# Kernel optimization log

Hardware: AMD Instinct MI355X
Metric: run time of the kernel (lower is better)

The kernel has to match this reference:

```python
import jax, jax.numpy as jnp
import numpy as np

EMBED_DIM = 192
NUM_HEADS = 4
HEAD_DIM = EMBED_DIM // NUM_HEADS
SCALE = HEAD_DIM ** -0.5


def setup_inputs() -> dict:
    key = jax.random.key(0)
    k_x, k_wqkv, k_bqkv, k_wp, k_bp = jax.random.split(key, 5)
    B, P, N, d = 8, 4, 1024, EMBED_DIM
    x = jax.random.normal(k_x, (B, P, N, d), dtype=jnp.float32)
    # torch Linear: y = x @ W.T + b, W shape [out, in]
    w_qkv = jax.random.normal(k_wqkv, (3 * d, d), dtype=jnp.float32) * (d ** -0.5)
    b_qkv = jax.random.normal(k_bqkv, (3 * d,), dtype=jnp.float32) * 0.02
    w_proj = jax.random.normal(k_wp, (d, d), dtype=jnp.float32) * (d ** -0.5)
    b_proj = jax.random.normal(k_bp, (d,), dtype=jnp.float32) * 0.02
    return {"x": x, "w_qkv": w_qkv, "b_qkv": b_qkv, "w_proj": w_proj, "b_proj": b_proj}


def reference(x, w_qkv, b_qkv, w_proj, b_proj):
    B, P, N, d = x.shape
    H, D = NUM_HEADS, HEAD_DIM
    qkv = jnp.einsum('bpnd,ed->bpne', x, w_qkv) + b_qkv  # [B,P,N,3d]
    q, k, v = jnp.split(qkv, 3, axis=-1)
    # split heads -> [B,P,H,N,D]
    split = lambda t: t.reshape(B, P, N, H, D).transpose(0, 1, 3, 2, 4)
    q, k, v = split(q), split(k), split(v)
    attn = jnp.einsum('bphnd,bphmd->bphnm', q, k) * SCALE
    attn = jax.nn.softmax(attn, axis=-1)
    z = jnp.einsum('bphnm,bphmd->bphnd', attn, v)
    z = z.transpose(0, 1, 3, 2, 4).reshape(B, P, N, H * D)
    z = jnp.einsum('bpnd,ed->bpne', z, w_proj) + b_proj
    return z
```

## Files before the change

### kernel.cpp

```cpp
#include <hip/hip_runtime.h>
#include <hip/hip_bf16.h>
#include <cstdint>
#include <cstddef>

typedef __attribute__((ext_vector_type(8))) short bf16x8;
typedef __attribute__((ext_vector_type(4))) float floatx4;
typedef __attribute__((ext_vector_type(16))) float floatx16;

#define SCALE_L2E 0.20823560929138437f

#define BPH 128
#define SEQ 1024
#define DMODEL 192
#define DHEAD 48
#define MROWS 32768
#define RESCALE_THR 11.5f

#define ZERO16 {0.f,0.f,0.f,0.f,0.f,0.f,0.f,0.f,0.f,0.f,0.f,0.f,0.f,0.f,0.f,0.f}

__device__ __forceinline__ unsigned short bfu(float f) {
    return __bfloat16_as_ushort(__float2bfloat16(f));
}
__device__ __forceinline__ unsigned pk2(float lo, float hi) {
    return (unsigned)bfu(lo) | ((unsigned)bfu(hi) << 16);
}

__global__ __launch_bounds__(256) void qkv_kernel(
    const float* __restrict__ x,
    const float* __restrict__ w_qkv,
    const float* __restrict__ b_qkv,
    unsigned short* __restrict__ q_ws,
    unsigned short* __restrict__ k_ws,
    unsigned short* __restrict__ vt_ws)
{
    __shared__ unsigned short a_lds[64 * 200];
    __shared__ unsigned short w_lds[64 * 200];
    const int t = threadIdx.x;
    const int m0 = blockIdx.x * 64;
    const int n0 = blockIdx.y * 64;

    #pragma unroll
    for (int i = 0; i < 12; ++i) {
        int idx = t + i * 256;
        int row = idx / 48, c4 = idx % 48;
        float4 v = *reinterpret_cast<const float4*>(x + (size_t)(m0 + row) * DMODEL + c4 * 4);
        unsigned short* dst = &a_lds[row * 200 + c4 * 4];
        dst[0] = bfu(v.x); dst[1] = bfu(v.y); dst[2] = bfu(v.z); dst[3] = bfu(v.w);
    }
    #pragma unroll
    for (int i = 0; i < 12; ++i) {
        int idx = t + i * 256;
        int row = idx / 48, c4 = idx % 48;
        float4 v = *reinterpret_cast<const float4*>(w_qkv + (size_t)(n0 + row) * DMODEL + c4 * 4);
        unsigned short* dst = &w_lds[row * 200 + c4 * 4];
        dst[0] = bfu(v.x); dst[1] = bfu(v.y); dst[2] = bfu(v.z); dst[3] = bfu(v.w);
    }
    __syncthreads();

    const int lane = t & 63, w = t >> 6;
    const int lrow = lane & 15, lhi = lane >> 4;

    floatx4 zf = {0.f, 0.f, 0.f, 0.f};
    floatx4 acc[4] = {zf, zf, zf, zf};

    #pragma unroll
    for (int ks = 0; ks < 6; ++ks) {
        bf16x8 af = *reinterpret_cast<const bf16x8*>(&a_lds[(w * 16 + lrow) * 200 + ks * 32 + lhi * 8]);
        #pragma unroll
        for (int cb = 0; cb < 4; ++cb) {
            bf16x8 bfr = *reinterpret_cast<const bf16x8*>(&w_lds[(cb * 16 + lrow) * 200 + ks * 32 + lhi * 8]);
            acc[cb] = __builtin_amdgcn_mfma_f32_16x16x32_bf16(af, bfr, acc[cb], 0, 0, 0);
        }
    }

    const int sec = n0 / 192;
    if (sec == 2) {
        __syncthreads();
        #pragma unroll
        for (int cb = 0; cb < 4; ++cb) {
            float bias = b_qkv[n0 + cb * 16 + lrow];
            #pragma unroll
            for (int r = 0; r < 4; ++r)
                a_lds[(cb * 16 + lrow) * 72 + (w * 16 + lhi * 4 + r)] = bfu(acc[cb][r] + bias);
        }
        __syncthreads();
        const int bp = m0 >> 10, nb = m0 & 1023;
        #pragma unroll
        for (int i = 0; i < 2; ++i) {
            int ch = t + i * 256;
            int c_local = ch >> 3, seg = ch & 7;
            int cc = n0 + c_local - 384;
            int h = cc / 48, dd = cc - h * 48;
            *reinterpret_cast<bf16x8*>(
                &vt_ws[((size_t)(bp * 4 + h) * DHEAD + dd) * SEQ + nb + seg * 8]) =
                *reinterpret_cast<const bf16x8*>(&a_lds[c_local * 72 + seg * 8]);
        }
    } else {
        #pragma unroll
        for (int cb = 0; cb < 4; ++cb) {
            int c = n0 + cb * 16 + lrow;
            int cc = c - sec * 192;
            int h = cc / 48, dd = cc - h * 48;
            float bias = b_qkv[c];
            #pragma unroll
            for (int r = 0; r < 4; ++r) {
                int m = m0 + w * 16 + lhi * 4 + r;
                float val = acc[cb][r] + bias;
                int bp = m >> 10, n = m & 1023;
                int bph = bp * 4 + h;
                if (sec == 0) {
                    q_ws[((size_t)bph * SEQ + n) * DHEAD + dd] = bfu(val * SCALE_L2E);
                } else {
                    k_ws[((size_t)bph * SEQ + n) * DHEAD + dd] = bfu(val);
                }
            }
        }
    }
}

__global__ __launch_bounds__(256, 4) void attn_kernel(
    const unsigned short* __restrict__ q_ws,
    const unsigned short* __restrict__ k_ws,
    const unsigned short* __restrict__ vt_ws,
    unsigned short* __restrict__ z_ws)
{
    const int t = threadIdx.x, lane = t & 63, w = t >> 6;
    const int q31 = lane & 31, hi = lane >> 5;
    const int d = blockIdx.x;
    const int bph = (d & 7) | ((d >> 6) << 3);
    const int qc = (d >> 3) & 7;
    const int q0 = qc * 128 + w * 32;
    const int bp = bph >> 2, h = bph & 3;

    bf16x8 qf[3];
    {
        const unsigned short* qp = q_ws + ((size_t)bph * SEQ + q0 + q31) * DHEAD + hi * 8;
        #pragma unroll
        for (int ks = 0; ks < 3; ++ks)
            qf[ks] = *reinterpret_cast<const bf16x8*>(qp + ks * 16);
    }

    const unsigned short* kp  = k_ws + ((size_t)bph * SEQ + q31) * DHEAD + hi * 8;
    const int vrow1 = (32 + q31 > 47) ? 47 : (32 + q31);
    const unsigned short* vp0 = vt_ws + ((size_t)bph * DHEAD + q31)  * (size_t)SEQ + hi * 8;
    const unsigned short* vp1 = vt_ws + ((size_t)bph * DHEAD + vrow1) * (size_t)SEQ + hi * 8;

    floatx16 oa0 = ZERO16, oa1 = ZERO16;
    float m_prev = -INFINITY, l_sum = 0.f;

    #pragma unroll 1
    for (int kt = 0; kt < 16; ++kt) {
        const int kt0 = kt * 64;

        const unsigned short* kpt = kp + (size_t)kt0 * DHEAD;
        bf16x8 kf[6], vf0[4], vf1[4];
        #pragma unroll
        for (int ks = 0; ks < 3; ++ks) {
            kf[ks]     = *reinterpret_cast<const bf16x8*>(kpt + ks * 16);
            kf[ks + 3] = *reinterpret_cast<const bf16x8*>(kpt + 32 * DHEAD + ks * 16);
        }
        #pragma unroll
        for (int ksv = 0; ksv < 4; ++ksv) {
            vf0[ksv] = *reinterpret_cast<const bf16x8*>(vp0 + kt0 + ksv * 16);
            vf1[ksv] = *reinterpret_cast<const bf16x8*>(vp1 + kt0 + ksv * 16);
        }

        floatx16 s0 = ZERO16, s1 = ZERO16;
        #pragma unroll
        for (int ks = 0; ks < 3; ++ks) {
            s0 = __builtin_amdgcn_mfma_f32_32x32x16_bf16(kf[ks],     qf[ks], s0, 0, 0, 0);
            s1 = __builtin_amdgcn_mfma_f32_32x32x16_bf16(kf[ks + 3], qf[ks], s1, 0, 0, 0);
        }

        float tmax = fmaxf(s0[0], s1[0]);
        #pragma unroll
        for (int r = 1; r < 16; ++r) tmax = fmaxf(tmax, fmaxf(s0[r], s1[r]));
        tmax = fmaxf(tmax, __shfl_xor(tmax, 32, 64));
        if (!__all((int)(tmax <= m_prev + RESCALE_THR))) {
            const float mnew = fmaxf(m_prev, tmax);
            const float scale = exp2f(m_prev - mnew);
            m_prev = mnew;
            l_sum *= scale;
            oa0 = oa0 * scale;
            oa1 = oa1 * scale;
        }
        const float mref = m_prev;

        float ts = 0.f;
        #pragma unroll
        for (int kvb = 0; kvb < 2; ++kvb) {
            unsigned W[8], X[8];
            #pragma unroll
            for (int u = 0; u < 8; ++u) {
                float e0 = __builtin_amdgcn_exp2f((kvb ? s1[2*u]   : s0[2*u])   - mref);
                float e1 = __builtin_amdgcn_exp2f((kvb ? s1[2*u+1] : s0[2*u+1]) - mref);
                ts += e0 + e1;
                W[u] = pk2(e0, e1);
                X[u] = __shfl_xor(W[u], 32, 64);
            }
            #pragma unroll
            for (int s = 0; s < 2; ++s) {
                const int a = s * 4;
                union { bf16x8 v; unsigned wd[4]; } pf;
                pf.wd[0] = hi ? X[a+2] : W[a];
                pf.wd[1] = hi ? X[a+3] : W[a+1];
                pf.wd[2] = hi ? W[a+2] : X[a];
                pf.wd[3] = hi ? W[a+3] : X[a+1];
                const int ksv = kvb * 2 + s;
                oa0 = __builtin_amdgcn_mfma_f32_32x32x16_bf16(vf0[ksv], pf.v, oa0, 0, 0, 0);
                oa1 = __builtin_amdgcn_mfma_f32_32x32x16_bf16(vf1[ksv], pf.v, oa1, 0, 0, 0);
            }
        }
        ts += __shfl_xor(ts, 32, 64);
        l_sum += ts;
    }

    const float inv = 1.0f / l_sum;
    unsigned* zp = reinterpret_cast<unsigned*>(
        z_ws + ((size_t)bp * SEQ + q0 + q31) * DMODEL + h * DHEAD);
    #pragma unroll
    for (int u = 0; u < 8; ++u) {
        int dd = 2 * (u & 1) + 8 * (u >> 1) + 4 * hi;
        zp[dd >> 1] = pk2(oa0[2*u] * inv, oa0[2*u+1] * inv);
    }
    #pragma unroll
    for (int u = 0; u < 4; ++u) {
        int dd = 32 + 2 * (u & 1) + 8 * (u >> 1) + 4 * hi;
        zp[dd >> 1] = pk2(oa1[2*u] * inv, oa1[2*u+1] * inv);
    }
}

__global__ __launch_bounds__(256) void proj_kernel(
    const unsigned short* __restrict__ z_ws,
    const float* __restrict__ w_proj,
    const float* __restrict__ b_proj,
    float* __restrict__ out)
{
    __shared__ unsigned short a_lds[64 * 200];
    __shared__ unsigned short w_lds[64 * 200];
    const int t = threadIdx.x;
    const int m0 = blockIdx.x * 64;
    const int n0 = blockIdx.y * 64;

    for (int i = t; i < 1536; i += 256) {
        int row = i / 24, c8 = i % 24;
        *reinterpret_cast<bf16x8*>(&a_lds[row * 200 + c8 * 8]) =
            *reinterpret_cast<const bf16x8*>(&z_ws[(size_t)(m0 + row) * DMODEL + c8 * 8]);
    }
    #pragma unroll
    for (int i = 0; i < 12; ++i) {
        int idx = t + i * 256;
        int row = idx / 48, c4 = idx % 48;
        float4 v = *reinterpret_cast<const float4*>(w_proj + (size_t)(n0 + row) * DMODEL + c4 * 4);
        unsigned short* dst = &w_lds[row * 200 + c4 * 4];
        dst[0] = bfu(v.x); dst[1] = bfu(v.y); dst[2] = bfu(v.z); dst[3] = bfu(v.w);
    }
    __syncthreads();

    const int lane = t & 63, w = t >> 6;
    const int lrow = lane & 15, lhi = lane >> 4;

    floatx4 zf = {0.f, 0.f, 0.f, 0.f};
    floatx4 acc[4] = {zf, zf, zf, zf};

    #pragma unroll
    for (int ks = 0; ks < 6; ++ks) {
        bf16x8 af = *reinterpret_cast<const bf16x8*>(&a_lds[(w * 16 + lrow) * 200 + ks * 32 + lhi * 8]);
        #pragma unroll
        for (int cb = 0; cb < 4; ++cb) {
            bf16x8 bfr = *reinterpret_cast<const bf16x8*>(&w_lds[(cb * 16 + lrow) * 200 + ks * 32 + lhi * 8]);
            acc[cb] = __builtin_amdgcn_mfma_f32_16x16x32_bf16(af, bfr, acc[cb], 0, 0, 0);
        }
    }

    #pragma unroll
    for (int cb = 0; cb < 4; ++cb) {
        int c = n0 + cb * 16 + lrow;
        float bias = b_proj[c];
        #pragma unroll
        for (int r = 0; r < 4; ++r) {
            int m = m0 + w * 16 + lhi * 4 + r;
            out[(size_t)m * DMODEL + c] = acc[cb][r] + bias;
        }
    }
}

extern "C" void kernel_launch(void* const* d_in, const int* in_sizes, int n_in,
                              void* d_out, int out_size, void* d_ws, size_t ws_size,
                              hipStream_t stream) {
    const float* x      = (const float*)d_in[0];
    const float* w_qkv  = (const float*)d_in[1];
    const float* b_qkv  = (const float*)d_in[2];
    const float* w_proj = (const float*)d_in[3];
    const float* b_proj = (const float*)d_in[4];
    float* out = (float*)d_out;

    unsigned short* q_ws  = (unsigned short*)d_ws;
    unsigned short* k_ws  = q_ws  + (size_t)BPH * SEQ * DHEAD;
    unsigned short* vt_ws = k_ws  + (size_t)BPH * SEQ * DHEAD;
    unsigned short* z_ws  = vt_ws + (size_t)BPH * DHEAD * SEQ;

    qkv_kernel<<<dim3(512, 9), 256, 0, stream>>>(x, w_qkv, b_qkv, q_ws, k_ws, vt_ws);
    attn_kernel<<<1024, 256, 0, stream>>>(q_ws, k_ws, vt_ws, z_ws);
    proj_kernel<<<dim3(512, 3), 256, 0, stream>>>(z_ws, w_proj, b_proj, out);
}
```

Before: 111.1 us.

## Prefetch next K tile, split V loads, add MFMA priority, vectorize LDS stores

The attention loop now loads the next K tile's fragments into registers right after the QK MFMAs, and defers the second V half load until after them. This lets global loads overlap with the softmax and MFMA work. It also raises wave priority around the MFMA blocks, restructures the max reduction into a tree, and splits exp/shuffle/MFMA phases. Separately, the GEMM kernels pack bf16 pairs into a single 8-byte LDS store instead of four 2-byte stores. These changes add register pressure and a wrap-around prefetch of the first tile on the last iteration.

Measured after the change: 197.3 us. 1.78x slower.

```diff
diff --git a/kernel.cpp b/kernel.cpp
--- a/kernel.cpp
+++ b/kernel.cpp
@@ -6,6 +6,7 @@
 typedef __attribute__((ext_vector_type(8))) short bf16x8;
 typedef __attribute__((ext_vector_type(4))) float floatx4;
 typedef __attribute__((ext_vector_type(16))) float floatx16;
+typedef __attribute__((ext_vector_type(2))) unsigned uintx2;
 
 #define SCALE_L2E 0.20823560929138437f
 
@@ -44,16 +45,16 @@
         int idx = t + i * 256;
         int row = idx / 48, c4 = idx % 48;
         float4 v = *reinterpret_cast<const float4*>(x + (size_t)(m0 + row) * DMODEL + c4 * 4);
-        unsigned short* dst = &a_lds[row * 200 + c4 * 4];
-        dst[0] = bfu(v.x); dst[1] = bfu(v.y); dst[2] = bfu(v.z); dst[3] = bfu(v.w);
+        uintx2 p; p.x = pk2(v.x, v.y); p.y = pk2(v.z, v.w);
+        *reinterpret_cast<uintx2*>(&a_lds[row * 200 + c4 * 4]) = p;
     }
     #pragma unroll
     for (int i = 0; i < 12; ++i) {
         int idx = t + i * 256;
         int row = idx / 48, c4 = idx % 48;
         float4 v = *reinterpret_cast<const float4*>(w_qkv + (size_t)(n0 + row) * DMODEL + c4 * 4);
-        unsigned short* dst = &w_lds[row * 200 + c4 * 4];
-        dst[0] = bfu(v.x); dst[1] = bfu(v.y); dst[2] = bfu(v.z); dst[3] = bfu(v.w);
+        uintx2 p; p.x = pk2(v.x, v.y); p.y = pk2(v.z, v.w);
+        *reinterpret_cast<uintx2*>(&w_lds[row * 200 + c4 * 4]) = p;
     }
     __syncthreads();
 
@@ -148,34 +149,54 @@
     floatx16 oa0 = ZERO16, oa1 = ZERO16;
     float m_prev = -INFINITY, l_sum = 0.f;
 
+    bf16x8 kf[6];
+    #pragma unroll
+    for (int ks = 0; ks < 3; ++ks) {
+        kf[ks]     = *reinterpret_cast<const bf16x8*>(kp + ks * 16);
+        kf[ks + 3] = *reinterpret_cast<const bf16x8*>(kp + 32 * DHEAD + ks * 16);
+    }
+
     #pragma unroll 1
     for (int kt = 0; kt < 16; ++kt) {
         const int kt0 = kt * 64;
 
-        const unsigned short* kpt = kp + (size_t)kt0 * DHEAD;
-        bf16x8 kf[6], vf0[4], vf1[4];
-        #pragma unroll
-        for (int ks = 0; ks < 3; ++ks) {
-            kf[ks]     = *reinterpret_cast<const bf16x8*>(kpt + ks * 16);
-            kf[ks + 3] = *reinterpret_cast<const bf16x8*>(kpt + 32 * DHEAD + ks * 16);
-        }
-        #pragma unroll
-        for (int ksv = 0; ksv < 4; ++ksv) {
+        bf16x8 vf0[4];
+        #pragma unroll
+        for (int ksv = 0; ksv < 4; ++ksv)
             vf0[ksv] = *reinterpret_cast<const bf16x8*>(vp0 + kt0 + ksv * 16);
-            vf1[ksv] = *reinterpret_cast<const bf16x8*>(vp1 + kt0 + ksv * 16);
-        }
 
         floatx16 s0 = ZERO16, s1 = ZERO16;
+        __builtin_amdgcn_s_setprio(1);
         #pragma unroll
         for (int ks = 0; ks < 3; ++ks) {
             s0 = __builtin_amdgcn_mfma_f32_32x32x16_bf16(kf[ks],     qf[ks], s0, 0, 0, 0);
             s1 = __builtin_amdgcn_mfma_f32_32x32x16_bf16(kf[ks + 3], qf[ks], s1, 0, 0, 0);
         }
-
-        float tmax = fmaxf(s0[0], s1[0]);
-        #pragma unroll
-        for (int r = 1; r < 16; ++r) tmax = fmaxf(tmax, fmaxf(s0[r], s1[r]));
+        __builtin_amdgcn_s_setprio(0);
+
+        {
+            const unsigned short* kpn = kp + (size_t)(((kt + 1) & 15) * 64) * DHEAD;
+            #pragma unroll
+            for (int ks = 0; ks < 3; ++ks) {
+                kf[ks]     = *reinterpret_cast<const bf16x8*>(kpn + ks * 16);
+                kf[ks + 3] = *reinterpret_cast<const bf16x8*>(kpn + 32 * DHEAD + ks * 16);
+            }
+        }
+
+        bf16x8 vf1[4];
+        #pragma unroll
+        for (int ksv = 0; ksv < 4; ++ksv)
+            vf1[ksv] = *reinterpret_cast<const bf16x8*>(vp1 + kt0 + ksv * 16);
+
+        float a[8];
+        #pragma unroll
+        for (int u = 0; u < 8; ++u)
+            a[u] = fmaxf(fmaxf(s0[2*u], s0[2*u+1]), fmaxf(s1[2*u], s1[2*u+1]));
+        float m01 = fmaxf(fmaxf(a[0], a[1]), fmaxf(a[2], a[3]));
+        float m23 = fmaxf(fmaxf(a[4], a[5]), fmaxf(a[6], a[7]));
+        float tmax = fmaxf(m01, m23);
         tmax = fmaxf(tmax, __shfl_xor(tmax, 32, 64));
+
         if (!__all((int)(tmax <= m_prev + RESCALE_THR))) {
             const float mnew = fmaxf(m_prev, tmax);
             const float scale = exp2f(m_prev - mnew);
@@ -186,33 +207,71 @@
         }
         const float mref = m_prev;
 
-        float ts = 0.f;
-        #pragma unroll
-        for (int kvb = 0; kvb < 2; ++kvb) {
-            unsigned W[8], X[8];
-            #pragma unroll
-            for (int u = 0; u < 8; ++u) {
-                float e0 = __builtin_amdgcn_exp2f((kvb ? s1[2*u]   : s0[2*u])   - mref);
-                float e1 = __builtin_amdgcn_exp2f((kvb ? s1[2*u+1] : s0[2*u+1]) - mref);
-                ts += e0 + e1;
-                W[u] = pk2(e0, e1);
-                X[u] = __shfl_xor(W[u], 32, 64);
-            }
-            #pragma unroll
-            for (int s = 0; s < 2; ++s) {
-                const int a = s * 4;
-                union { bf16x8 v; unsigned wd[4]; } pf;
-                pf.wd[0] = hi ? X[a+2] : W[a];
-                pf.wd[1] = hi ? X[a+3] : W[a+1];
-                pf.wd[2] = hi ? W[a+2] : X[a];
-                pf.wd[3] = hi ? W[a+3] : X[a+1];
-                const int ksv = kvb * 2 + s;
-                oa0 = __builtin_amdgcn_mfma_f32_32x32x16_bf16(vf0[ksv], pf.v, oa0, 0, 0, 0);
-                oa1 = __builtin_amdgcn_mfma_f32_32x32x16_bf16(vf1[ksv], pf.v, oa1, 0, 0, 0);
-            }
-        }
+        unsigned W0[8], W1[8];
+        float tsA = 0.f, tsB = 0.f;
+        #pragma unroll
+        for (int u = 0; u < 8; ++u) {
+            float e0 = __builtin_amdgcn_exp2f(s0[2*u]   - mref);
+            float e1 = __builtin_amdgcn_exp2f(s0[2*u+1] - mref);
+            tsA += e0 + e1;
+            W0[u] = pk2(e0, e1);
+        }
+        #pragma unroll
+        for (int u = 0; u < 8; ++u) {
+            float e0 = __builtin_amdgcn_exp2f(s1[2*u]   - mref);
+            float e1 = __builtin_amdgcn_exp2f(s1[2*u+1] - mref);
+            tsB += e0 + e1;
+            W1[u] = pk2(e0, e1);
+        }
+        float ts = tsA + tsB;
         ts += __shfl_xor(ts, 32, 64);
         l_sum += ts;
+
+        unsigned X0[8], X1[8];
+        #pragma unroll
+        for (int u = 0; u < 8; ++u) X0[u] = __shfl_xor(W0[u], 32, 64);
+        #pragma unroll
+        for (int u = 0; u < 8; ++u) X1[u] = __shfl_xor(W1[u], 32, 64);
+
+        union U { bf16x8 v; unsigned wd[4]; };
+        __builtin_amdgcn_s_setprio(1);
+        {
+            U pa;
+            pa.wd[0] = hi ? X0[2] : W0[0];
+            pa.wd[1] = hi ? X0[3] : W0[1];
+            pa.wd[2] = hi ? W0[2] : X0[0];
+            pa.wd[3] = hi ? W0[3] : X0[1];
+            oa0 = __builtin_amdgcn_mfma_f32_32x32x16_bf16(vf0[0], pa.v, oa0, 0, 0, 0);
+            oa1 = __builtin_amdgcn_mfma_f32_32x32x16_bf16(vf1[0], pa.v, oa1, 0, 0, 0);
+        }
+        {
+            U pb;
+            pb.wd[0] = hi ? X0[6] : W0[4];
+            pb.wd[1] = hi ? X0[7] : W0[5];
+            pb.wd[2] = hi ? W0[6] : X0[4];
+            pb.wd[3] = hi ? W0[7] : X0[5];
+            oa0 = __builtin_amdgcn_mfma_f32_32x32x16_bf16(vf0[1], pb.v, oa0, 0, 0, 0);
+            oa1 = __builtin_amdgcn_mfma_f32_32x32x16_bf16(vf1[1], pb.v, oa1, 0, 0, 0);
+        }
+        {
+            U pc;
+            pc.wd[0] = hi ? X1[2] : W1[0];
+            pc.wd[1] = hi ? X1[3] : W1[1];
+            pc.wd[2] = hi ? W1[2] : X1[0];
+            pc.wd[3] = hi ? W1[3] : X1[1];
+            oa0 = __builtin_amdgcn_mfma_f32_32x32x16_bf16(vf0[2], pc.v, oa0, 0, 0, 0);
+            oa1 = __builtin_amdgcn_mfma_f32_32x32x16_bf16(vf1[2], pc.v, oa1, 0, 0, 0);
+        }
+        {
+            U pd;
+            pd.wd[0] = hi ? X1[6] : W1[4];
+            pd.wd[1] = hi ? X1[7] : W1[5];
+            pd.wd[2] = hi ? W1[6] : X1[4];
+            pd.wd[3] = hi ? W1[7] : X1[5];
+            oa0 = __builtin_amdgcn_mfma_f32_32x32x16_bf16(vf0[3], pd.v, oa0, 0, 0, 0);
+            oa1 = __builtin_amdgcn_mfma_f32_32x32x16_bf16(vf1[3], pd.v, oa1, 0, 0, 0);
+        }
+        __builtin_amdgcn_s_setprio(0);
     }
 
     const float inv = 1.0f / l_sum;
@@ -252,8 +311,8 @@
         int idx = t + i * 256;
         int row = idx / 48, c4 = idx % 48;
         float4 v = *reinterpret_cast<const float4*>(w_proj + (size_t)(n0 + row) * DMODEL + c4 * 4);
-        unsigned short* dst = &w_lds[row * 200 + c4 * 4];
-        dst[0] = bfu(v.x); dst[1] = bfu(v.y); dst[2] = bfu(v.z); dst[3] = bfu(v.w);
+        uintx2 p; p.x = pk2(v.x, v.y); p.y = pk2(v.z, v.w);
+        *reinterpret_cast<uintx2*>(&w_lds[row * 200 + c4 * 4]) = p;
     }
     __syncthreads();
 
```
